# Performance work log

Measured on AMD Instinct MI355X. Metric: run time of the kernel, lower is better.

Reference implementation:

```python
import jax, jax.numpy as jnp
import numpy as np

B, T, I, H = 64, 1024, 1024, 1024


def setup_inputs() -> dict:
    key = jax.random.key(0)
    k1, k2, k3, k4, k5 = jax.random.split(key, 5)
    s_i = 1.0 / np.sqrt(I)
    s_h = 1.0 / np.sqrt(H)
    return {
        "input": jax.random.normal(k1, (B, T, I), dtype=jnp.float32),
        "hidden": jnp.zeros((B, H), dtype=jnp.float32),
        "W_ih": jax.random.uniform(k2, (H, I), jnp.float32, -s_i, s_i),
        "b_ih": jax.random.uniform(k3, (H,), jnp.float32, -s_i, s_i),
        "W_hh": jax.random.uniform(k4, (H, H), jnp.float32, -s_h, s_h),
        "b_hh": jax.random.uniform(k5, (H,), jnp.float32, -s_h, s_h),
    }


def reference(input, hidden, W_ih, b_ih, W_hh, b_hh):
    # Precompute the input projection for all timesteps in one big GEMM:
    # x_proj[b, t, h] = input @ W_ih^T + b_ih  (same math as per-step Linear)
    x_proj = jnp.einsum("bti,hi->bth", input, W_ih) + b_ih + b_hh

    def step(h, xp_t):
        h_new = jnp.tanh(xp_t + h @ W_hh.T)
        return h_new, h_new

    # scan over time: xp has shape (T, B, H)
    h_last, outs = jax.lax.scan(step, hidden, jnp.swapaxes(x_proj, 0, 1))
    output = jnp.swapaxes(outs, 0, 1)  # (B, T, H)
    return output, h_last
```

## Files before the change

### kernel.cpp

```cpp
#include <hip/hip_runtime.h>
#include <hip/hip_bf16.h>

#define TDIM 1024
#define HDIM 1024
#define IDIM 1024
#define BSZ  64

typedef __attribute__((ext_vector_type(4))) float  floatx4;
typedef __attribute__((ext_vector_type(2))) float  floatx2;
typedef __attribute__((ext_vector_type(8))) short  shortx8;

static __device__ __forceinline__ short f2bf(float x) {
    unsigned u = __builtin_bit_cast(unsigned, x);
    u += 0x7fffu + ((u >> 16) & 1u);
    return (short)(u >> 16);
}

static __device__ __forceinline__ shortx8 pack8(floatx4 a, floatx4 b) {
    shortx8 r;
    r[0] = f2bf(a[0]); r[1] = f2bf(a[1]); r[2] = f2bf(a[2]); r[3] = f2bf(a[3]);
    r[4] = f2bf(b[0]); r[5] = f2bf(b[1]); r[6] = f2bf(b[2]); r[7] = f2bf(b[3]);
    return r;
}

static __device__ __forceinline__ unsigned ld_flag(const unsigned* p) {
    unsigned v;
    asm volatile("global_load_dword %0, %1, off sc0 sc1" : "=v"(v) : "v"(p) : "memory");
    asm volatile("s_waitcnt vmcnt(0)" ::: "memory");
    return v;
}
static __device__ __forceinline__ unsigned ld_h(const unsigned* p) {
    unsigned v;
    asm volatile("global_load_dword %0, %1, off sc0 sc1" : "=v"(v) : "v"(p) : "memory");
    return v;
}
static __device__ __forceinline__ void st_h(unsigned short* p, unsigned short v) {
    asm volatile("global_store_short %0, %1, off sc0 sc1" :: "v"(p), "v"(v) : "memory");
}
static __device__ __forceinline__ void st_flag(unsigned* p, unsigned v) {
    asm volatile("global_store_dword %0, %1, off sc0 sc1" :: "v"(p), "v"(v) : "memory");
}

__global__ __launch_bounds__(256, 2)
void xp_gemm(const float* __restrict__ A, const float* __restrict__ W,
             const float* __restrict__ bih, const float* __restrict__ bhh,
             float* __restrict__ out)
{
    __shared__ short As[128 * 72];
    __shared__ short Bs[128 * 72];

    const int tid  = threadIdx.x;
    const int bx   = blockIdx.x;
    const int m0   = (bx >> 3) * 128;
    const int n0   = (bx & 7) * 128;
    const int lane = tid & 63;
    const int w    = tid >> 6;
    const int wm   = w & 1, wn = w >> 1;
    const int col  = lane & 15, quad = lane >> 4;

    const int srow = tid >> 1;
    const int scol = (tid & 1) * 32;
    const float* ap = A + (size_t)(m0 + srow) * IDIM + scol;
    const float* wp = W + (size_t)(n0 + srow) * IDIM + scol;
    short* asw = As + srow * 72 + scol;
    short* bsw = Bs + srow * 72 + scol;

    floatx4 acc[4][4];
#pragma unroll
    for (int i = 0; i < 4; i++)
#pragma unroll
        for (int j = 0; j < 4; j++) acc[i][j] = (floatx4){0.f, 0.f, 0.f, 0.f};

    for (int kt = 0; kt < IDIM; kt += 64) {
        floatx4 av[8], bv[8];
        const floatx4* pa = (const floatx4*)(ap + kt);
        const floatx4* pb = (const floatx4*)(wp + kt);
#pragma unroll
        for (int q = 0; q < 8; q++) { av[q] = pa[q]; bv[q] = pb[q]; }
        __syncthreads();
#pragma unroll
        for (int q = 0; q < 4; q++) {
            *(shortx8*)(asw + q * 8) = pack8(av[2 * q], av[2 * q + 1]);
            *(shortx8*)(bsw + q * 8) = pack8(bv[2 * q], bv[2 * q + 1]);
        }
        __syncthreads();
#pragma unroll
        for (int kb = 0; kb < 64; kb += 32) {
            shortx8 af[4], bf[4];
#pragma unroll
            for (int i = 0; i < 4; i++)
                af[i] = *(const shortx8*)(As + (wm * 64 + i * 16 + col) * 72 + kb + quad * 8);
#pragma unroll
            for (int j = 0; j < 4; j++)
                bf[j] = *(const shortx8*)(Bs + (wn * 64 + j * 16 + col) * 72 + kb + quad * 8);
#pragma unroll
            for (int i = 0; i < 4; i++)
#pragma unroll
                for (int j = 0; j < 4; j++)
                    acc[i][j] = __builtin_amdgcn_mfma_f32_16x16x32_bf16(af[i], bf[j], acc[i][j], 0, 0, 0);
        }
    }

#pragma unroll
    for (int j = 0; j < 4; j++) {
        const int n = n0 + wn * 64 + j * 16 + col;
        const float bias = bih[n] + bhh[n];
#pragma unroll
        for (int i = 0; i < 4; i++) {
            const int mb = m0 + wm * 64 + i * 16 + quad * 4;
#pragma unroll
            for (int r = 0; r < 4; r++)
                out[(size_t)(mb + r) * HDIM + n] = acc[i][j][r] + bias;
        }
    }
}

__global__ __launch_bounds__(512, 1)
void rnn_rec(float* __restrict__ out,
             const float* __restrict__ Whh, const float* __restrict__ h0,
             unsigned short* __restrict__ hexch, unsigned* __restrict__ flags)
{
    __shared__ short hlds[16 * 1032];

    const int tid  = threadIdx.x;
    const int g    = blockIdx.x >> 3;
    const int role = blockIdx.x & 7;
    const int lane = tid & 63;
    const int w    = tid >> 6;
    const int col  = lane & 15, quad = lane >> 4;
    const int nglob = role * 128 + w * 16 + col;
    const int b0   = quad * 4;

    {
        unsigned* z = (unsigned*)(hlds + 8 * 1032);
        for (int i = tid; i < 4 * 1032; i += 512) z[i] = 0u;
    }

    shortx8 bfrag[32];
    {
        const float* wrow = Whh + (size_t)nglob * HDIM + quad * 8;
#pragma unroll
        for (int kb = 0; kb < 32; kb++) {
            const floatx4* p = (const floatx4*)(wrow + kb * 32);
            bfrag[kb] = pack8(p[0], p[1]);
        }
    }
    __syncthreads();

    const int bsafe = b0 & 7;
    float xp[4], xpn[4];
#pragma unroll
    for (int r = 0; r < 4; r++)
        xp[r] = __builtin_nontemporal_load(
            out + (size_t)(g * 8 + bsafe + r) * (TDIM * HDIM) + nglob);

    const int cc = w * 128 + lane * 2;
    const unsigned* fpoll = flags + (size_t)g * 64 + (size_t)w * 8;
    unsigned*       fpub  = flags + (size_t)g * 64 + (size_t)role * 8 + w;

    for (int t = 0; t < TDIM; ++t) {
        if (t == 0) {
            const int c2 = tid * 2;
#pragma unroll
            for (int j = 0; j < 8; j++) {
                floatx2 f = *(const floatx2*)(h0 + (size_t)(g * 8 + j) * HDIM + c2);
                const unsigned pk = (unsigned)(unsigned short)f2bf(f[0]) |
                                    ((unsigned)(unsigned short)f2bf(f[1]) << 16);
                *(unsigned*)(hlds + j * 1032 + c2) = pk;
            }
        } else {
            int guard = 0;
            for (;;) {
                const unsigned f = ld_flag(fpoll + (lane & 7));
                if (__all((int)(f >= (unsigned)t))) break;
                if (++guard > (1 << 16)) break;
                asm volatile("s_sleep 1");
            }
            const unsigned short* base =
                hexch + (size_t)(t & 1) * (8 * 8 * 1024) + (size_t)g * (8 * 1024) + cc;
            unsigned hv[8];
#pragma unroll
            for (int j = 0; j < 8; j++)
                hv[j] = ld_h((const unsigned*)(base + j * 1024));
            asm volatile("s_waitcnt vmcnt(0)" ::: "memory");
            __builtin_amdgcn_sched_barrier(0);
#pragma unroll
            for (int j = 0; j < 8; j++)
                *(unsigned*)(hlds + j * 1032 + cc) = hv[j];
        }

        asm volatile("s_waitcnt lgkmcnt(0)" ::: "memory");
        __builtin_amdgcn_s_barrier();

        floatx4 a0 = (floatx4){0.f, 0.f, 0.f, 0.f};
        floatx4 a1 = a0, a2 = a0, a3 = a0;
#pragma unroll
        for (int kb = 0; kb < 32; kb += 4) {
            shortx8 f0 = *(const shortx8*)(hlds + col * 1032 + (kb + 0) * 32 + quad * 8);
            shortx8 f1 = *(const shortx8*)(hlds + col * 1032 + (kb + 1) * 32 + quad * 8);
            shortx8 f2 = *(const shortx8*)(hlds + col * 1032 + (kb + 2) * 32 + quad * 8);
            shortx8 f3 = *(const shortx8*)(hlds + col * 1032 + (kb + 3) * 32 + quad * 8);
            a0 = __builtin_amdgcn_mfma_f32_16x16x32_bf16(f0, bfrag[kb + 0], a0, 0, 0, 0);
            a1 = __builtin_amdgcn_mfma_f32_16x16x32_bf16(f1, bfrag[kb + 1], a1, 0, 0, 0);
            a2 = __builtin_amdgcn_mfma_f32_16x16x32_bf16(f2, bfrag[kb + 2], a2, 0, 0, 0);
            a3 = __builtin_amdgcn_mfma_f32_16x16x32_bf16(f3, bfrag[kb + 3], a3, 0, 0, 0);
        }
        floatx4 acc = (a0 + a1) + (a2 + a3);

        float hval[4];
#pragma unroll
        for (int r = 0; r < 4; r++)
            hval[r] = tanhf(xp[r] + acc[r]);

        if (t + 1 < TDIM) {
            if (b0 < 8) {
                unsigned short* hd =
                    hexch + (size_t)((t + 1) & 1) * (8 * 8 * 1024) + (size_t)g * (8 * 1024);
#pragma unroll
                for (int r = 0; r < 4; r++)
                    st_h(hd + (size_t)(b0 + r) * 1024 + nglob,
                         (unsigned short)f2bf(hval[r]));
            }
            asm volatile("s_waitcnt vmcnt(0)" ::: "memory");
            if (lane == 0) st_flag(fpub, (unsigned)(t + 1));
        }

        if (b0 < 8) {
#pragma unroll
            for (int r = 0; r < 4; r++) {
                const int b = g * 8 + b0 + r;
                const size_t oidx = (size_t)b * (TDIM * HDIM) + (size_t)t * HDIM + nglob;
                __builtin_nontemporal_store(hval[r], out + oidx);
                if (t == TDIM - 1)
                    out[(size_t)BSZ * TDIM * HDIM + (size_t)b * HDIM + nglob] = hval[r];
            }
        }
        if (t + 1 < TDIM) {
#pragma unroll
            for (int r = 0; r < 4; r++)
                xpn[r] = __builtin_nontemporal_load(
                    out + (size_t)(g * 8 + bsafe + r) * (TDIM * HDIM) + (size_t)(t + 1) * HDIM + nglob);
#pragma unroll
            for (int r = 0; r < 4; r++) xp[r] = xpn[r];
        }

        if (t + 1 < TDIM) {
            asm volatile("s_waitcnt lgkmcnt(0)" ::: "memory");
            __builtin_amdgcn_s_barrier();
        }
    }
}

extern "C" void kernel_launch(void* const* d_in, const int* in_sizes, int n_in,
                              void* d_out, int out_size, void* d_ws, size_t ws_size,
                              hipStream_t stream)
{
    const float* input = (const float*)d_in[0];
    const float* h0    = (const float*)d_in[1];
    const float* W_ih  = (const float*)d_in[2];
    const float* b_ih  = (const float*)d_in[3];
    const float* W_hh  = (const float*)d_in[4];
    const float* b_hh  = (const float*)d_in[5];
    float* out = (float*)d_out;

    char* ws = (char*)d_ws;
    unsigned*       flags = (unsigned*)ws;
    unsigned short* hexch = (unsigned short*)(ws + 16384);

    hipMemsetAsync(ws, 0, 16384, stream);

    xp_gemm<<<dim3(4096), dim3(256), 0, stream>>>(input, W_ih, b_ih, b_hh, out);
    rnn_rec<<<dim3(64),   dim3(512), 0, stream>>>(out, W_hh, h0, hexch, flags);
}
```

Before: 4.385 ms.

## Replace flag-based handoff with step-tagged hidden-state words polled directly

Each hidden-state value is now stored as a 32-bit word that packs the bf16 value with the timestep tag. Consumers poll the data itself until every tag matches, which removes the separate flag store, the vmcnt wait before publishing, and the extra load round trip after the flag is seen. The next-step xp prefetch is moved ahead of the matmul, and output stores are no longer nontemporal. In exchange the exchange buffer doubles in size, and each poll reads more bytes.

```diff
diff --git a/kernel.cpp b/kernel.cpp
--- a/kernel.cpp
+++ b/kernel.cpp
@@ -23,21 +23,13 @@
     return r;
 }
 
-static __device__ __forceinline__ unsigned ld_flag(const unsigned* p) {
-    unsigned v;
-    asm volatile("global_load_dword %0, %1, off sc0 sc1" : "=v"(v) : "v"(p) : "memory");
-    asm volatile("s_waitcnt vmcnt(0)" ::: "memory");
+static __device__ __forceinline__ unsigned long long ld_mall8(const unsigned* p) {
+    unsigned long long v;
+    asm volatile("global_load_dwordx2 %0, %1, off sc0 sc1"
+                 : "=v"(v) : "v"(p) : "memory");
     return v;
 }
-static __device__ __forceinline__ unsigned ld_h(const unsigned* p) {
-    unsigned v;
-    asm volatile("global_load_dword %0, %1, off sc0 sc1" : "=v"(v) : "v"(p) : "memory");
-    return v;
-}
-static __device__ __forceinline__ void st_h(unsigned short* p, unsigned short v) {
-    asm volatile("global_store_short %0, %1, off sc0 sc1" :: "v"(p), "v"(v) : "memory");
-}
-static __device__ __forceinline__ void st_flag(unsigned* p, unsigned v) {
+static __device__ __forceinline__ void st_tag(unsigned* p, unsigned v) {
     asm volatile("global_store_dword %0, %1, off sc0 sc1" :: "v"(p), "v"(v) : "memory");
 }
 
@@ -118,7 +110,7 @@
 __global__ __launch_bounds__(512, 1)
 void rnn_rec(float* __restrict__ out,
              const float* __restrict__ Whh, const float* __restrict__ h0,
-             unsigned short* __restrict__ hexch, unsigned* __restrict__ flags)
+             unsigned* __restrict__ hexch)
 {
     __shared__ short hlds[16 * 1032];
 
@@ -155,8 +147,7 @@
             out + (size_t)(g * 8 + bsafe + r) * (TDIM * HDIM) + nglob);
 
     const int cc = w * 128 + lane * 2;
-    const unsigned* fpoll = flags + (size_t)g * 64 + (size_t)w * 8;
-    unsigned*       fpub  = flags + (size_t)g * 64 + (size_t)role * 8 + w;
+    const unsigned gbase = (unsigned)(g * 8192 + cc);
 
     for (int t = 0; t < TDIM; ++t) {
         if (t == 0) {
@@ -169,24 +160,39 @@
                 *(unsigned*)(hlds + j * 1032 + c2) = pk;
             }
         } else {
+            const unsigned long long msk = 0x0000FFFF0000FFFFULL;
+            const unsigned long long tt  = (unsigned long long)(unsigned)t;
+            const unsigned long long pat = tt | (tt << 32);
+            const unsigned* base = hexch + ((unsigned)(t & 1) << 16) + gbase;
+            unsigned long long hv[8];
             int guard = 0;
             for (;;) {
-                const unsigned f = ld_flag(fpoll + (lane & 7));
-                if (__all((int)(f >= (unsigned)t))) break;
+#pragma unroll
+                for (int j = 0; j < 8; j++)
+                    hv[j] = ld_mall8(base + (size_t)j * 1024);
+                asm volatile("s_waitcnt vmcnt(0)" ::: "memory");
+                __builtin_amdgcn_sched_barrier(0);
+                bool bad = false;
+#pragma unroll
+                for (int j = 0; j < 8; j++)
+                    bad |= ((hv[j] & msk) != pat);
+                if (!__any((int)bad)) break;
                 if (++guard > (1 << 16)) break;
                 asm volatile("s_sleep 1");
             }
-            const unsigned short* base =
-                hexch + (size_t)(t & 1) * (8 * 8 * 1024) + (size_t)g * (8 * 1024) + cc;
-            unsigned hv[8];
-#pragma unroll
-            for (int j = 0; j < 8; j++)
-                hv[j] = ld_h((const unsigned*)(base + j * 1024));
-            asm volatile("s_waitcnt vmcnt(0)" ::: "memory");
-            __builtin_amdgcn_sched_barrier(0);
-#pragma unroll
-            for (int j = 0; j < 8; j++)
-                *(unsigned*)(hlds + j * 1032 + cc) = hv[j];
+#pragma unroll
+            for (int j = 0; j < 8; j++) {
+                const unsigned pk = (unsigned)((hv[j] >> 16) & 0xFFFFu) |
+                                    (unsigned)((hv[j] >> 32) & 0xFFFF0000u);
+                *(unsigned*)(hlds + j * 1032 + cc) = pk;
+            }
+        }
+
+        if (t + 1 < TDIM) {
+#pragma unroll
+            for (int r = 0; r < 4; r++)
+                xpn[r] = __builtin_nontemporal_load(
+                    out + (size_t)(g * 8 + bsafe + r) * (TDIM * HDIM) + (size_t)(t + 1) * HDIM + nglob);
         }
 
         asm volatile("s_waitcnt lgkmcnt(0)" ::: "memory");
@@ -213,16 +219,14 @@
             hval[r] = tanhf(xp[r] + acc[r]);
 
         if (t + 1 < TDIM) {
+            unsigned* hd = hexch + ((unsigned)((t + 1) & 1) << 16) + (unsigned)(g * 8192);
+            const unsigned tag = (unsigned)(t + 1);
             if (b0 < 8) {
-                unsigned short* hd =
-                    hexch + (size_t)((t + 1) & 1) * (8 * 8 * 1024) + (size_t)g * (8 * 1024);
 #pragma unroll
                 for (int r = 0; r < 4; r++)
-                    st_h(hd + (size_t)(b0 + r) * 1024 + nglob,
-                         (unsigned short)f2bf(hval[r]));
-            }
-            asm volatile("s_waitcnt vmcnt(0)" ::: "memory");
-            if (lane == 0) st_flag(fpub, (unsigned)(t + 1));
+                    st_tag(hd + (size_t)(b0 + r) * 1024 + nglob,
+                           ((unsigned)(unsigned short)f2bf(hval[r]) << 16) | tag);
+            }
         }
 
         if (b0 < 8) {
@@ -230,19 +234,13 @@
             for (int r = 0; r < 4; r++) {
                 const int b = g * 8 + b0 + r;
                 const size_t oidx = (size_t)b * (TDIM * HDIM) + (size_t)t * HDIM + nglob;
-                __builtin_nontemporal_store(hval[r], out + oidx);
+                out[oidx] = hval[r];
                 if (t == TDIM - 1)
                     out[(size_t)BSZ * TDIM * HDIM + (size_t)b * HDIM + nglob] = hval[r];
             }
         }
-        if (t + 1 < TDIM) {
-#pragma unroll
-            for (int r = 0; r < 4; r++)
-                xpn[r] = __builtin_nontemporal_load(
-                    out + (size_t)(g * 8 + bsafe + r) * (TDIM * HDIM) + (size_t)(t + 1) * HDIM + nglob);
-#pragma unroll
-            for (int r = 0; r < 4; r++) xp[r] = xpn[r];
-        }
+#pragma unroll
+        for (int r = 0; r < 4; r++) xp[r] = xpn[r];
 
         if (t + 1 < TDIM) {
             asm volatile("s_waitcnt lgkmcnt(0)" ::: "memory");
@@ -263,12 +261,10 @@
     const float* b_hh  = (const float*)d_in[5];
     float* out = (float*)d_out;
 
-    char* ws = (char*)d_ws;
-    unsigned*       flags = (unsigned*)ws;
-    unsigned short* hexch = (unsigned short*)(ws + 16384);
-
-    hipMemsetAsync(ws, 0, 16384, stream);
+    unsigned* hexch = (unsigned*)d_ws;
+
+    hipMemsetAsync(hexch, 0, (size_t)2 * 65536 * 4, stream);
 
     xp_gemm<<<dim3(4096), dim3(256), 0, stream>>>(input, W_ih, b_ih, b_hh, out);
-    rnn_rec<<<dim3(64),   dim3(512), 0, stream>>>(out, W_hh, h0, hexch, flags);
-}
+    rnn_rec<<<dim3(64),   dim3(512), 0, stream>>>(out, W_hh, h0, hexch);
+}
```

After: 3.865 ms. 11.9% less time.
